# Performance work log

Hardware: AMD Instinct MI355X
Metric: run time of the kernel (lower is better)

## Reference

```python
import jax, jax.numpy as jnp
import numpy as np

N = 16384          # tokens (batch*seq)
D = 2048           # input_dim
H = 2 * D          # router hidden dim
E = 64             # num_experts
NUM_SHARED = 8
TOP_K = 2


def setup_inputs() -> dict:
    key = jax.random.key(0)
    k_x, k_w1, k_b1, k_w2, k_b2 = jax.random.split(key, 5)
    s1 = 1.0 / np.sqrt(D)
    s2 = 1.0 / np.sqrt(H)
    return {
        "x": jax.random.normal(k_x, (N, D), dtype=jnp.float32),
        "W1": jax.random.uniform(k_w1, (D, H), jnp.float32, -s1, s1),
        "b1": jax.random.uniform(k_b1, (H,), jnp.float32, -s1, s1),
        "W2": jax.random.uniform(k_w2, (H, E), jnp.float32, -s2, s2),
        "b2": jax.random.uniform(k_b2, (E,), jnp.float32, -s2, s2),
    }


def reference(x, W1, b1, W2, b2):
    # router MLP: linear -> exact (erf) GELU -> linear -> softmax
    h = jax.nn.gelu(x @ W1 + b1, approximate=False)          # [N, H]
    weights = jax.nn.softmax(h @ W2 + b2, axis=-1)            # [N, E]
    global_weights = weights[:, :NUM_SHARED]                  # [N, num_shared]
    local = weights[:, NUM_SHARED:]                           # [N, E - num_shared]
    local_weights, local_indices = jax.lax.top_k(local, TOP_K)  # [N, top_k] each
    return (global_weights, local_weights, local_indices, weights)
```

## Files before the change

### kernel.cpp

```cpp
#include <hip/hip_runtime.h>
#include <math.h>

namespace {
constexpr int kN = 16384;
constexpr int kD = 2048;
constexpr int kH = 4096;
constexpr int kE = 64;
constexpr int kShared = 8;

constexpr int OFF_GW = 0;
constexpr int OFF_LW = kN * kShared;
constexpr int OFF_LI = OFF_LW + kN * 2;
constexpr int OFF_W  = OFF_LI + kN * 2;

constexpr int GS_STRIDE = 132;
constexpr int HSPLIT = 4;
constexpr int CHUNKS = 8;

constexpr size_t XH_OFF  = 0;
constexpr size_t XL_OFF  = (size_t)kN * kD;
constexpr size_t W1TH_OFF = XL_OFF + (size_t)kN * kD;
constexpr size_t W1TL_OFF = W1TH_OFF + (size_t)kH * kD;
constexpr size_t WS_BASE = (W1TL_OFF + (size_t)kH * kD) * 2;
constexpr size_t PART_FLOAT_OFF = WS_BASE / 4;
constexpr size_t WS_FULL = WS_BASE + (size_t)HSPLIT * kN * kE * 4;

constexpr int BUF_FLOATS = 64 * GS_STRIDE;
constexpr int BUF_F16    = BUF_FLOATS * 2;

constexpr int CXB = 8192;
}

typedef _Float16 half8  __attribute__((ext_vector_type(8)));
typedef _Float16 half4t __attribute__((ext_vector_type(4)));
typedef float    f32x16 __attribute__((ext_vector_type(16)));

__device__ __forceinline__ void async16(const _Float16* g, _Float16* l) {
    __builtin_amdgcn_global_load_lds(
        (const __attribute__((address_space(1))) void*)g,
        (__attribute__((address_space(3))) void*)l, 16, 0, 0);
}

__global__ __launch_bounds__(256)
void convert_xw(const float* __restrict__ x, _Float16* __restrict__ xh,
                _Float16* __restrict__ xl,
                const float* __restrict__ W1, _Float16* __restrict__ th,
                _Float16* __restrict__ tl)
{
    __shared__ float T[64][65];
    const int b = blockIdx.x;
    const int t = threadIdx.x;

    if (b < CXB) {
        #pragma unroll
        for (int it = 0; it < 4; ++it) {
            const size_t i = (((size_t)it * CXB + b) * 256 + t) * 4;
            const float4 v = *reinterpret_cast<const float4*>(x + i);
            half4t h, l;
            const float vs[4] = {v.x, v.y, v.z, v.w};
            #pragma unroll
            for (int j = 0; j < 4; ++j) {
                const _Float16 hj = (_Float16)vs[j];
                h[j] = hj;
                l[j] = (_Float16)((vs[j] - (float)hj) * 2048.0f);
            }
            *reinterpret_cast<half4t*>(xh + i) = h;
            *reinterpret_cast<half4t*>(xl + i) = l;
        }
        return;
    }

    const int bb = b - CXB;
    const int bk = bb & 31;
    const int bn = bb >> 5;
    const int k0 = bk * 64, n0 = bn * 64;
    const int c4 = (t & 15) * 4, r = t >> 4;

    #pragma unroll
    for (int i = 0; i < 4; ++i) {
        const int kk = r + 16 * i;
        const float4 v = *reinterpret_cast<const float4*>(
            W1 + (size_t)(k0 + kk) * kH + n0 + c4);
        T[kk][c4 + 0] = v.x; T[kk][c4 + 1] = v.y;
        T[kk][c4 + 2] = v.z; T[kk][c4 + 3] = v.w;
    }
    __syncthreads();
    #pragma unroll
    for (int i = 0; i < 4; ++i) {
        const int nn = r + 16 * i;
        half4t h, l;
        #pragma unroll
        for (int j = 0; j < 4; ++j) {
            const float vv = T[c4 + j][nn];
            const _Float16 hj = (_Float16)vv;
            h[j] = hj;
            l[j] = (_Float16)((vv - (float)hj) * 2048.0f);
        }
        *reinterpret_cast<half4t*>(th + (size_t)(n0 + nn) * kD + k0 + c4) = h;
        *reinterpret_cast<half4t*>(tl + (size_t)(n0 + nn) * kD + k0 + c4) = l;
    }
}

__global__ __launch_bounds__(256, 2)
void gemm1_mfma(const _Float16* __restrict__ xh, const float* __restrict__ b1,
                const float* __restrict__ W2, float* __restrict__ dst,
                int atomicMode)
{
    __shared__ __align__(16) float smem[2 * BUF_FLOATS];

    const int t = threadIdx.x;
    const int lane = t & 63;
    const int w = t >> 6;
    const int bx = blockIdx.x;
    const int xcd = bx & 7;
    const int j8 = bx >> 3;
    const int hSplit = 2 * (xcd & 1) + (j8 & 1);
    const int rowBlock = (xcd >> 1) * 32 + (j8 >> 1);
    const int rowBase = rowBlock * 128;

    const int mw = (w >> 1) * 64;
    const int nc32 = (w & 1) * 32;

    unsigned int gofsA[4], gofsB[4];
    #pragma unroll
    for (int i = 0; i < 8; ++i) {
        const int c = i * 256 + t;
        const int tile = c >> 9;
        const int s = c & 511;
        const int row = s >> 2;
        const int pq = s & 3;
        const int q = pq ^ (row & 3) ^ ((row >> 2) & 3);
        const unsigned int plane =
            (tile == 0) ? (unsigned int)XH_OFF :
            (tile == 1) ? (unsigned int)XL_OFF :
            (tile == 2) ? (unsigned int)W1TH_OFF : (unsigned int)W1TL_OFF;
        if (tile < 2)
            gofsA[i] = plane + (unsigned int)(rowBase + row) * kD + q * 8;
        else
            gofsB[i - 4] = plane + (unsigned int)row * kD + q * 8;
    }

    int aOff[2][2], bOff[2][2];
    #pragma unroll
    for (int mt = 0; mt < 2; ++mt)
        #pragma unroll
        for (int ks = 0; ks < 2; ++ks) {
            const int row = mw + mt * 32 + (lane & 31);
            const int q = (lane >> 5) + 2 * ks;
            aOff[mt][ks] = row * 32 + ((q ^ (row & 3) ^ ((row >> 2) & 3)) * 8);
        }
    #pragma unroll
    for (int nt = 0; nt < 2; ++nt)
        #pragma unroll
        for (int ks = 0; ks < 2; ++ks) {
            const int row = nt * 64 + nc32 + (lane & 31);
            const int q = (lane >> 5) + 2 * ks;
            bOff[nt][ks] = row * 32 + ((q ^ (row & 3) ^ ((row >> 2) & 3)) * 8);
        }

    const int g_r0 = (t >> 3) * 4;
    const int g_e0 = (t & 7) * 8;
    float lacc[4][8];
    #pragma unroll
    for (int i = 0; i < 4; ++i)
        #pragma unroll
        for (int j = 0; j < 8; ++j) lacc[i][j] = 0.0f;

    auto stageA = [&](int buf, int nk) {
        _Float16* l = (_Float16*)smem + (size_t)buf * BUF_F16;
        #pragma unroll
        for (int i = 0; i < 4; ++i)
            async16(xh + gofsA[i] + nk, l + ((i * 256 + t) * 8));
    };
    auto stageB = [&](int buf, int nc, int nk) {
        _Float16* l = (_Float16*)smem + (size_t)buf * BUF_F16;
        const unsigned int hOff =
            (unsigned int)(hSplit * (CHUNKS * 128) + nc * 128) * kD;
        #pragma unroll
        for (int i = 0; i < 4; ++i)
            async16(xh + gofsB[i] + hOff + nk, l + (((i + 4) * 256 + t) * 8));
    };

    int cur = 0;
    stageA(0, 0);
    stageB(0, 0, 0);

    for (int chunk = 0; chunk < CHUNKS; ++chunk) {
        const int hBase = hSplit * (CHUNKS * 128) + chunk * 128;

        f32x16 accH[2][2], accL[2][2];
        #pragma unroll
        for (int a = 0; a < 2; ++a)
            #pragma unroll
            for (int b = 0; b < 2; ++b)
                #pragma unroll
                for (int r = 0; r < 16; ++r) { accH[a][b][r] = 0.0f; accL[a][b][r] = 0.0f; }

        for (int kt = 0; kt < kD; kt += 32) {
            const bool isLast = (chunk == CHUNKS - 1) && (kt == kD - 32);
            int nc = chunk, nk = kt + 32;
            if (nk == kD) { nc = chunk + 1; nk = 0; }

            const _Float16* lds = (const _Float16*)smem + (size_t)cur * BUF_F16;
            const int nbuf = cur ^ 1;

            if (!isLast) {
                stageA(nbuf, nk);
                asm volatile("s_waitcnt vmcnt(4)" ::: "memory");
            } else {
                asm volatile("s_waitcnt vmcnt(0)" ::: "memory");
            }
            __builtin_amdgcn_s_barrier();
            asm volatile("" ::: "memory");

            {
                half8 aH[2], aL[2], bH[2], bL[2];
                #pragma unroll
                for (int mt = 0; mt < 2; ++mt) {
                    aH[mt] = *reinterpret_cast<const half8*>(lds + aOff[mt][0]);
                    aL[mt] = *reinterpret_cast<const half8*>(lds + 4096 + aOff[mt][0]);
                }
                #pragma unroll
                for (int nt = 0; nt < 2; ++nt) {
                    bH[nt] = *reinterpret_cast<const half8*>(lds + 8192 + bOff[nt][0]);
                    bL[nt] = *reinterpret_cast<const half8*>(lds + 12288 + bOff[nt][0]);
                }
                if (!isLast) stageB(nbuf, nc, nk);
                __builtin_amdgcn_s_setprio(1);
                #pragma unroll
                for (int mt = 0; mt < 2; ++mt)
                    #pragma unroll
                    for (int nt = 0; nt < 2; ++nt) {
                        accH[mt][nt] = __builtin_amdgcn_mfma_f32_32x32x16_f16(
                            aH[mt], bH[nt], accH[mt][nt], 0, 0, 0);
                        accL[mt][nt] = __builtin_amdgcn_mfma_f32_32x32x16_f16(
                            aH[mt], bL[nt], accL[mt][nt], 0, 0, 0);
                        accL[mt][nt] = __builtin_amdgcn_mfma_f32_32x32x16_f16(
                            aL[mt], bH[nt], accL[mt][nt], 0, 0, 0);
                    }
                __builtin_amdgcn_s_setprio(0);
                __builtin_amdgcn_sched_barrier(0);
            }
            asm volatile("" ::: "memory");
            __builtin_amdgcn_s_barrier();
            asm volatile("" ::: "memory");

            {
                half8 aH[2], aL[2], bH[2], bL[2];
                #pragma unroll
                for (int mt = 0; mt < 2; ++mt) {
                    aH[mt] = *reinterpret_cast<const half8*>(lds + aOff[mt][1]);
                    aL[mt] = *reinterpret_cast<const half8*>(lds + 4096 + aOff[mt][1]);
                }
                #pragma unroll
                for (int nt = 0; nt < 2; ++nt) {
                    bH[nt] = *reinterpret_cast<const half8*>(lds + 8192 + bOff[nt][1]);
                    bL[nt] = *reinterpret_cast<const half8*>(lds + 12288 + bOff[nt][1]);
                }
                __builtin_amdgcn_s_setprio(1);
                #pragma unroll
                for (int mt = 0; mt < 2; ++mt)
                    #pragma unroll
                    for (int nt = 0; nt < 2; ++nt) {
                        accH[mt][nt] = __builtin_amdgcn_mfma_f32_32x32x16_f16(
                            aH[mt], bH[nt], accH[mt][nt], 0, 0, 0);
                        accL[mt][nt] = __builtin_amdgcn_mfma_f32_32x32x16_f16(
                            aH[mt], bL[nt], accL[mt][nt], 0, 0, 0);
                        accL[mt][nt] = __builtin_amdgcn_mfma_f32_32x32x16_f16(
                            aL[mt], bH[nt], accL[mt][nt], 0, 0, 0);
                    }
                __builtin_amdgcn_s_setprio(0);
                __builtin_amdgcn_sched_barrier(0);
            }
            asm volatile("s_waitcnt lgkmcnt(0)" ::: "memory");
            __builtin_amdgcn_s_barrier();
            asm volatile("" ::: "memory");
            cur ^= 1;
        }

        float* gS = smem + (size_t)(cur ^ 1) * BUF_FLOATS;
        const float inv2048 = 1.0f / 2048.0f;
        const int hl = nc32 + (lane & 31);
        for (int hf = 0; hf < 2; ++hf) {
            if (hf) {
                asm volatile("s_waitcnt lgkmcnt(0)" ::: "memory");
                __builtin_amdgcn_s_barrier();
                asm volatile("" ::: "memory");
            }
            const float bb = b1[hBase + hf * 64 + hl];
            #pragma unroll
            for (int mt = 0; mt < 2; ++mt) {
                #pragma unroll
                for (int rq = 0; rq < 4; ++rq) {
                    float vr[4];
                    #pragma unroll
                    for (int rr = 0; rr < 4; ++rr) {
                        const int r = rq * 4 + rr;
                        const float hv = accH[mt][hf][r] + accL[mt][hf][r] * inv2048 + bb;
                        vr[rr] = 0.5f * hv * (1.0f + erff(hv * 0.70710678118654752f));
                    }
                    const int mrow = mw + mt * 32 + 8 * rq + 4 * (lane >> 5);
                    *reinterpret_cast<float4*>(gS + hl * GS_STRIDE + mrow) =
                        make_float4(vr[0], vr[1], vr[2], vr[3]);
                }
            }
            asm volatile("s_waitcnt lgkmcnt(0)" ::: "memory");
            __builtin_amdgcn_s_barrier();
            asm volatile("" ::: "memory");
            const float* W2p = W2 + (size_t)(hBase + hf * 64) * kE + g_e0;
            #pragma unroll 4
            for (int h = 0; h < 64; ++h) {
                const float4 gv = *reinterpret_cast<const float4*>(gS + h * GS_STRIDE + g_r0);
                const float4 w0 = *reinterpret_cast<const float4*>(W2p + (size_t)h * kE);
                const float4 w1 = *reinterpret_cast<const float4*>(W2p + (size_t)h * kE + 4);
                const float ga[4] = {gv.x, gv.y, gv.z, gv.w};
                const float wb[8] = {w0.x, w0.y, w0.z, w0.w, w1.x, w1.y, w1.z, w1.w};
                #pragma unroll
                for (int i = 0; i < 4; ++i)
                    #pragma unroll
                    for (int j = 0; j < 8; ++j)
                        lacc[i][j] = fmaf(ga[i], wb[j], lacc[i][j]);
            }
        }
        asm volatile("s_waitcnt lgkmcnt(0)" ::: "memory");
        __builtin_amdgcn_s_barrier();
        asm volatile("" ::: "memory");
    }

    if (atomicMode) {
        #pragma unroll
        for (int i = 0; i < 4; ++i)
            #pragma unroll
            for (int j = 0; j < 8; ++j)
                atomicAdd(dst + (size_t)(rowBase + g_r0 + i) * kE + g_e0 + j, lacc[i][j]);
    } else {
        float* drow = dst + ((size_t)hSplit * kN + rowBase + g_r0) * kE + g_e0;
        #pragma unroll
        for (int i = 0; i < 4; ++i) {
            *reinterpret_cast<float4*>(drow + (size_t)i * kE) =
                make_float4(lacc[i][0], lacc[i][1], lacc[i][2], lacc[i][3]);
            *reinterpret_cast<float4*>(drow + (size_t)i * kE + 4) =
                make_float4(lacc[i][4], lacc[i][5], lacc[i][6], lacc[i][7]);
        }
    }
}

__global__ __launch_bounds__(256, 2)
void gemm1_kernel(const float* __restrict__ x, const float* __restrict__ W1,
                  const float* __restrict__ b1, const float* __restrict__ W2,
                  float* __restrict__ logits)
{
    __shared__ __align__(16) float smem[64 * GS_STRIDE];
    float* As = smem;
    float* Bs = smem + 32 * 128;
    float* gS = smem;

    const int t  = threadIdx.x;
    const int bx = blockIdx.x;
    const int rowBlock = bx >> 2;
    const int hSplit   = bx & 3;
    const int rowBase  = rowBlock * 128;
    const int hBase0   = hSplit * 1024;

    const int ty = t >> 4;
    const int tx = t & 15;
    const int r0 = ty * 8;
    const int c0 = tx * 8;
    const int g_r0 = (t >> 3) * 4;
    const int g_e0 = (t & 7) * 8;

    float lacc[4][8];
    #pragma unroll
    for (int i = 0; i < 4; ++i)
        #pragma unroll
        for (int j = 0; j < 8; ++j) lacc[i][j] = 0.0f;

    for (int chunk = 0; chunk < 8; ++chunk) {
        const int hBase = hBase0 + chunk * 128;
        float C[8][8];
        #pragma unroll
        for (int i = 0; i < 8; ++i)
            #pragma unroll
            for (int j = 0; j < 8; ++j) C[i][j] = 0.0f;

        for (int kt = 0; kt < kD; kt += 32) {
            __syncthreads();
            #pragma unroll
            for (int i = 0; i < 4; ++i) {
                const int f  = t + 256 * i;
                const int m  = f >> 3;
                const int kq = (f & 7) * 4;
                const float4 v = *reinterpret_cast<const float4*>(
                    x + (size_t)(rowBase + m) * kD + kt + kq);
                As[(kq + 0) * 128 + m] = v.x;
                As[(kq + 1) * 128 + m] = v.y;
                As[(kq + 2) * 128 + m] = v.z;
                As[(kq + 3) * 128 + m] = v.w;
            }
            #pragma unroll
            for (int i = 0; i < 4; ++i) {
                const int f  = t + 256 * i;
                const int k  = f >> 5;
                const int n4 = (f & 31) * 4;
                *reinterpret_cast<float4*>(Bs + k * 128 + n4) =
                    *reinterpret_cast<const float4*>(W1 + (size_t)(kt + k) * kH + hBase + n4);
            }
            __syncthreads();
            #pragma unroll 8
            for (int k = 0; k < 32; ++k) {
                const float4 a0 = *reinterpret_cast<const float4*>(As + k * 128 + r0);
                const float4 a1 = *reinterpret_cast<const float4*>(As + k * 128 + r0 + 4);
                const float4 b0 = *reinterpret_cast<const float4*>(Bs + k * 128 + c0);
                const float4 b1v = *reinterpret_cast<const float4*>(Bs + k * 128 + c0 + 4);
                const float a[8] = {a0.x, a0.y, a0.z, a0.w, a1.x, a1.y, a1.z, a1.w};
                const float b[8] = {b0.x, b0.y, b0.z, b0.w, b1v.x, b1v.y, b1v.z, b1v.w};
                #pragma unroll
                for (int i = 0; i < 8; ++i)
                    #pragma unroll
                    for (int j = 0; j < 8; ++j)
                        C[i][j] = fmaf(a[i], b[j], C[i][j]);
            }
        }

        #pragma unroll
        for (int j = 0; j < 8; ++j) {
            const float bb = b1[hBase + c0 + j];
            #pragma unroll
            for (int i = 0; i < 8; ++i) {
                const float hv = C[i][j] + bb;
                C[i][j] = 0.5f * hv * (1.0f + erff(hv * 0.70710678118654752f));
            }
        }

        for (int half = 0; half < 2; ++half) {
            __syncthreads();
            if ((tx >> 3) == half) {
                const int hloc0 = c0 - half * 64;
                #pragma unroll
                for (int j = 0; j < 8; ++j) {
                    const float4 col = make_float4(C[0][j], C[1][j], C[2][j], C[3][j]);
                    const float4 col2 = make_float4(C[4][j], C[5][j], C[6][j], C[7][j]);
                    *reinterpret_cast<float4*>(gS + (hloc0 + j) * GS_STRIDE + r0)     = col;
                    *reinterpret_cast<float4*>(gS + (hloc0 + j) * GS_STRIDE + r0 + 4) = col2;
                }
            }
            __syncthreads();
            const float* W2p = W2 + (size_t)(hBase + half * 64) * kE + g_e0;
            #pragma unroll 4
            for (int h = 0; h < 64; ++h) {
                const float4 gv = *reinterpret_cast<const float4*>(gS + h * GS_STRIDE + g_r0);
                const float4 w0 = *reinterpret_cast<const float4*>(W2p + (size_t)h * kE);
                const float4 w1 = *reinterpret_cast<const float4*>(W2p + (size_t)h * kE + 4);
                const float ga[4] = {gv.x, gv.y, gv.z, gv.w};
                const float wb[8] = {w0.x, w0.y, w0.z, w0.w, w1.x, w1.y, w1.z, w1.w};
                #pragma unroll
                for (int i = 0; i < 4; ++i)
                    #pragma unroll
                    for (int j = 0; j < 8; ++j)
                        lacc[i][j] = fmaf(ga[i], wb[j], lacc[i][j]);
            }
        }
    }

    #pragma unroll
    for (int i = 0; i < 4; ++i)
        #pragma unroll
        for (int j = 0; j < 8; ++j)
            atomicAdd(logits + (size_t)(rowBase + g_r0 + i) * kE + g_e0 + j, lacc[i][j]);
}

__global__ __launch_bounds__(256)
void router_kernel(const float* __restrict__ b2, const float* __restrict__ src,
                   int atomicMode, float* __restrict__ out)
{
    const int lane = threadIdx.x & 63;
    const int row  = blockIdx.x * 4 + (threadIdx.x >> 6);

    float logit;
    if (atomicMode) {
        logit = src[(size_t)row * kE + lane] + b2[lane];
    } else {
        const float* p = src + (size_t)row * kE + lane;
        logit = p[0] + p[(size_t)kN * kE] + p[(size_t)2 * kN * kE] +
                p[(size_t)3 * kN * kE] + b2[lane];
    }

    float m = logit;
    #pragma unroll
    for (int off = 32; off > 0; off >>= 1) m = fmaxf(m, __shfl_xor(m, off));
    const float p = expf(logit - m);
    float s = p;
    #pragma unroll
    for (int off = 32; off > 0; off >>= 1) s += __shfl_xor(s, off);
    const float w = p / s;

    out[OFF_W + (size_t)row * kE + lane] = w;
    if (lane < kShared) out[OFF_GW + (size_t)row * kShared + lane] = w;

    float v1 = (lane >= kShared) ? w : -1.0f;
    int   i1 = lane - kShared;
    #pragma unroll
    for (int off = 32; off > 0; off >>= 1) {
        const float ov = __shfl_xor(v1, off);
        const int   oi = __shfl_xor(i1, off);
        if (ov > v1 || (ov == v1 && oi < i1)) { v1 = ov; i1 = oi; }
    }
    float v2 = (lane >= kShared && (lane - kShared) != i1) ? w : -1.0f;
    int   i2 = lane - kShared;
    #pragma unroll
    for (int off = 32; off > 0; off >>= 1) {
        const float ov = __shfl_xor(v2, off);
        const int   oi = __shfl_xor(i2, off);
        if (ov > v2 || (ov == v2 && oi < i2)) { v2 = ov; i2 = oi; }
    }
    if (lane == 0) {
        out[OFF_LW + (size_t)row * 2 + 0] = v1;
        out[OFF_LW + (size_t)row * 2 + 1] = v2;
        out[OFF_LI + (size_t)row * 2 + 0] = (float)i1;
        out[OFF_LI + (size_t)row * 2 + 1] = (float)i2;
    }
}

extern "C" void kernel_launch(void* const* d_in, const int* in_sizes, int n_in,
                              void* d_out, int out_size, void* d_ws, size_t ws_size,
                              hipStream_t stream)
{
    const float* x  = (const float*)d_in[0];
    const float* W1 = (const float*)d_in[1];
    const float* b1 = (const float*)d_in[2];
    const float* W2 = (const float*)d_in[3];
    const float* b2 = (const float*)d_in[4];
    float* out = (float*)d_out;
    float* logits = out + OFF_W;

    if (ws_size >= WS_BASE) {
        _Float16* base = (_Float16*)d_ws;
        const int atomicMode = (ws_size >= WS_FULL) ? 0 : 1;
        float* dst = atomicMode ? logits : ((float*)d_ws + PART_FLOAT_OFF);
        if (atomicMode)
            hipMemsetAsync(logits, 0, (size_t)kN * kE * sizeof(float), stream);
        hipLaunchKernelGGL(convert_xw, dim3(CXB + (kD / 64) * (kH / 64)), dim3(256), 0, stream,
                           x, base + XH_OFF, base + XL_OFF,
                           W1, base + W1TH_OFF, base + W1TL_OFF);
        hipLaunchKernelGGL(gemm1_mfma, dim3((kN / 128) * HSPLIT), dim3(256), 0, stream,
                           base + XH_OFF, b1, W2, dst, atomicMode);
        hipLaunchKernelGGL(router_kernel, dim3(kN / 4), dim3(256), 0, stream,
                           b2, dst, atomicMode, out);
    } else {
        hipMemsetAsync(logits, 0, (size_t)kN * kE * sizeof(float), stream);
        hipLaunchKernelGGL(gemm1_kernel, dim3((kN / 128) * 4), dim3(256), 0, stream,
                           x, W1, b1, W2, logits);
        hipLaunchKernelGGL(router_kernel, dim3(kN / 4), dim3(256), 0, stream,
                           b2, logits, 1, out);
    }
}
```

Before: 1.225 ms.

## Add dedicated producer wave for async loads and merge split-fp16 accumulators

Adds a fifth wavefront per block that alone issues the async global-to-LDS loads for the double-buffered tiles, so the four compute waves only run MFMAs. The scaling of the split-fp16 operands moves so the hi*hi, hi*lo and lo*hi products all land at one scale, letting a single accumulator replace the separate high and low accumulators. This frees registers, and launch bounds move from 256 threads at 2 blocks to 320 threads at 3 blocks. The risks are that a single producer wave may not keep up with the load rate, and that the extra barrier per k-step and the changed precision scaling (hi scaled by 2048 in fp16, x lo unscaled) could cost throughput or accuracy.

```diff
diff --git a/kernel.cpp b/kernel.cpp
--- a/kernel.cpp
+++ b/kernel.cpp
@@ -62,7 +62,7 @@
             for (int j = 0; j < 4; ++j) {
                 const _Float16 hj = (_Float16)vs[j];
                 h[j] = hj;
-                l[j] = (_Float16)((vs[j] - (float)hj) * 2048.0f);
+                l[j] = (_Float16)(vs[j] - (float)hj);
             }
             *reinterpret_cast<half4t*>(xh + i) = h;
             *reinterpret_cast<half4t*>(xl + i) = l;
@@ -93,7 +93,7 @@
         for (int j = 0; j < 4; ++j) {
             const float vv = T[c4 + j][nn];
             const _Float16 hj = (_Float16)vv;
-            h[j] = hj;
+            h[j] = (_Float16)((float)hj * 2048.0f);
             l[j] = (_Float16)((vv - (float)hj) * 2048.0f);
         }
         *reinterpret_cast<half4t*>(th + (size_t)(n0 + nn) * kD + k0 + c4) = h;
@@ -101,7 +101,7 @@
     }
 }
 
-__global__ __launch_bounds__(256, 2)
+__global__ __launch_bounds__(320, 3)
 void gemm1_mfma(const _Float16* __restrict__ xh, const float* __restrict__ b1,
                 const float* __restrict__ W2, float* __restrict__ dst,
                 int atomicMode)
@@ -111,6 +111,7 @@
     const int t = threadIdx.x;
     const int lane = t & 63;
     const int w = t >> 6;
+    const bool producer = (w == 4);
     const int bx = blockIdx.x;
     const int xcd = bx & 7;
     const int j8 = bx >> 3;
@@ -121,25 +122,6 @@
     const int mw = (w >> 1) * 64;
     const int nc32 = (w & 1) * 32;
 
-    unsigned int gofsA[4], gofsB[4];
-    #pragma unroll
-    for (int i = 0; i < 8; ++i) {
-        const int c = i * 256 + t;
-        const int tile = c >> 9;
-        const int s = c & 511;
-        const int row = s >> 2;
-        const int pq = s & 3;
-        const int q = pq ^ (row & 3) ^ ((row >> 2) & 3);
-        const unsigned int plane =
-            (tile == 0) ? (unsigned int)XH_OFF :
-            (tile == 1) ? (unsigned int)XL_OFF :
-            (tile == 2) ? (unsigned int)W1TH_OFF : (unsigned int)W1TL_OFF;
-        if (tile < 2)
-            gofsA[i] = plane + (unsigned int)(rowBase + row) * kD + q * 8;
-        else
-            gofsB[i - 4] = plane + (unsigned int)row * kD + q * 8;
-    }
-
     int aOff[2][2], bOff[2][2];
     #pragma unroll
     for (int mt = 0; mt < 2; ++mt)
@@ -158,7 +140,7 @@
             bOff[nt][ks] = row * 32 + ((q ^ (row & 3) ^ ((row >> 2) & 3)) * 8);
         }
 
-    const int g_r0 = (t >> 3) * 4;
+    const int g_r0 = ((t & 255) >> 3) * 4;
     const int g_e0 = (t & 7) * 8;
     float lacc[4][8];
     #pragma unroll
@@ -166,160 +148,139 @@
         #pragma unroll
         for (int j = 0; j < 8; ++j) lacc[i][j] = 0.0f;
 
-    auto stageA = [&](int buf, int nk) {
+    const int pr0 = lane >> 2, ppq = lane & 3;
+    auto pstage = [&](int buf, int chunk, int kt) {
         _Float16* l = (_Float16*)smem + (size_t)buf * BUF_F16;
-        #pragma unroll
-        for (int i = 0; i < 4; ++i)
-            async16(xh + gofsA[i] + nk, l + ((i * 256 + t) * 8));
+        const int hBase = hSplit * (CHUNKS * 128) + chunk * 128;
+        #pragma clang loop unroll(disable)
+        for (int i = 0; i < 32; ++i) {
+            const int tile = i >> 3;
+            const int row = (i & 7) * 16 + pr0;
+            const int q = ppq ^ (row & 3) ^ ((row >> 2) & 3);
+            const unsigned int plane =
+                (tile == 0) ? (unsigned int)XH_OFF :
+                (tile == 1) ? (unsigned int)XL_OFF :
+                (tile == 2) ? (unsigned int)W1TH_OFF : (unsigned int)W1TL_OFF;
+            const unsigned int rsel = (tile < 2 ? rowBase : hBase) + row;
+            async16(xh + plane + rsel * (unsigned)kD + q * 8 + kt,
+                    l + ((i * 64 + lane) * 8));
+        }
     };
-    auto stageB = [&](int buf, int nc, int nk) {
-        _Float16* l = (_Float16*)smem + (size_t)buf * BUF_F16;
-        const unsigned int hOff =
-            (unsigned int)(hSplit * (CHUNKS * 128) + nc * 128) * kD;
-        #pragma unroll
-        for (int i = 0; i < 4; ++i)
-            async16(xh + gofsB[i] + hOff + nk, l + (((i + 4) * 256 + t) * 8));
-    };
-
-    int cur = 0;
-    stageA(0, 0);
-    stageB(0, 0, 0);
+
+    const float inv2048 = 1.0f / 2048.0f;
+    const int hl = nc32 + (lane & 31);
 
     for (int chunk = 0; chunk < CHUNKS; ++chunk) {
         const int hBase = hSplit * (CHUNKS * 128) + chunk * 128;
 
-        f32x16 accH[2][2], accL[2][2];
+        f32x16 acc[2][2];
         #pragma unroll
         for (int a = 0; a < 2; ++a)
             #pragma unroll
             for (int b = 0; b < 2; ++b)
                 #pragma unroll
-                for (int r = 0; r < 16; ++r) { accH[a][b][r] = 0.0f; accL[a][b][r] = 0.0f; }
-
-        for (int kt = 0; kt < kD; kt += 32) {
-            const bool isLast = (chunk == CHUNKS - 1) && (kt == kD - 32);
-            int nc = chunk, nk = kt + 32;
-            if (nk == kD) { nc = chunk + 1; nk = 0; }
-
-            const _Float16* lds = (const _Float16*)smem + (size_t)cur * BUF_F16;
-            const int nbuf = cur ^ 1;
-
-            if (!isLast) {
-                stageA(nbuf, nk);
-                asm volatile("s_waitcnt vmcnt(4)" ::: "memory");
-            } else {
-                asm volatile("s_waitcnt vmcnt(0)" ::: "memory");
-            }
-            __builtin_amdgcn_s_barrier();
-            asm volatile("" ::: "memory");
-
-            {
-                half8 aH[2], aL[2], bH[2], bL[2];
-                #pragma unroll
-                for (int mt = 0; mt < 2; ++mt) {
-                    aH[mt] = *reinterpret_cast<const half8*>(lds + aOff[mt][0]);
-                    aL[mt] = *reinterpret_cast<const half8*>(lds + 4096 + aOff[mt][0]);
-                }
-                #pragma unroll
-                for (int nt = 0; nt < 2; ++nt) {
-                    bH[nt] = *reinterpret_cast<const half8*>(lds + 8192 + bOff[nt][0]);
-                    bL[nt] = *reinterpret_cast<const half8*>(lds + 12288 + bOff[nt][0]);
-                }
-                if (!isLast) stageB(nbuf, nc, nk);
-                __builtin_amdgcn_s_setprio(1);
-                #pragma unroll
-                for (int mt = 0; mt < 2; ++mt)
-                    #pragma unroll
-                    for (int nt = 0; nt < 2; ++nt) {
-                        accH[mt][nt] = __builtin_amdgcn_mfma_f32_32x32x16_f16(
-                            aH[mt], bH[nt], accH[mt][nt], 0, 0, 0);
-                        accL[mt][nt] = __builtin_amdgcn_mfma_f32_32x32x16_f16(
-                            aH[mt], bL[nt], accL[mt][nt], 0, 0, 0);
-                        accL[mt][nt] = __builtin_amdgcn_mfma_f32_32x32x16_f16(
-                            aL[mt], bH[nt], accL[mt][nt], 0, 0, 0);
-                    }
-                __builtin_amdgcn_s_setprio(0);
-                __builtin_amdgcn_sched_barrier(0);
-            }
+                for (int r = 0; r < 16; ++r) acc[a][b][r] = 0.0f;
+
+        if (producer) {
+            pstage(0, chunk, 0);
+            pstage(1, chunk, 32);
+            asm volatile("s_waitcnt vmcnt(32)" ::: "memory");
+        }
+
+        for (int s = 0; s < 64; ++s) {
             asm volatile("" ::: "memory");
             __builtin_amdgcn_s_barrier();
             asm volatile("" ::: "memory");
 
-            {
-                half8 aH[2], aL[2], bH[2], bL[2];
-                #pragma unroll
-                for (int mt = 0; mt < 2; ++mt) {
-                    aH[mt] = *reinterpret_cast<const half8*>(lds + aOff[mt][1]);
-                    aL[mt] = *reinterpret_cast<const half8*>(lds + 4096 + aOff[mt][1]);
+            if (!producer) {
+                const _Float16* lds = (const _Float16*)smem + (size_t)(s & 1) * BUF_F16;
+                #pragma unroll
+                for (int ks = 0; ks < 2; ++ks) {
+                    half8 aH[2], aL[2], bH[2], bL[2];
+                    #pragma unroll
+                    for (int mt = 0; mt < 2; ++mt) {
+                        aH[mt] = *reinterpret_cast<const half8*>(lds + aOff[mt][ks]);
+                        aL[mt] = *reinterpret_cast<const half8*>(lds + 4096 + aOff[mt][ks]);
+                    }
+                    #pragma unroll
+                    for (int nt = 0; nt < 2; ++nt) {
+                        bH[nt] = *reinterpret_cast<const half8*>(lds + 8192 + bOff[nt][ks]);
+                        bL[nt] = *reinterpret_cast<const half8*>(lds + 12288 + bOff[nt][ks]);
+                    }
+                    __builtin_amdgcn_s_setprio(1);
+                    #pragma unroll
+                    for (int mt = 0; mt < 2; ++mt)
+                        #pragma unroll
+                        for (int nt = 0; nt < 2; ++nt) {
+                            acc[mt][nt] = __builtin_amdgcn_mfma_f32_32x32x16_f16(
+                                aH[mt], bH[nt], acc[mt][nt], 0, 0, 0);
+                            acc[mt][nt] = __builtin_amdgcn_mfma_f32_32x32x16_f16(
+                                aH[mt], bL[nt], acc[mt][nt], 0, 0, 0);
+                            acc[mt][nt] = __builtin_amdgcn_mfma_f32_32x32x16_f16(
+                                aL[mt], bH[nt], acc[mt][nt], 0, 0, 0);
+                        }
+                    __builtin_amdgcn_s_setprio(0);
                 }
-                #pragma unroll
-                for (int nt = 0; nt < 2; ++nt) {
-                    bH[nt] = *reinterpret_cast<const half8*>(lds + 8192 + bOff[nt][1]);
-                    bL[nt] = *reinterpret_cast<const half8*>(lds + 12288 + bOff[nt][1]);
-                }
-                __builtin_amdgcn_s_setprio(1);
-                #pragma unroll
-                for (int mt = 0; mt < 2; ++mt)
-                    #pragma unroll
-                    for (int nt = 0; nt < 2; ++nt) {
-                        accH[mt][nt] = __builtin_amdgcn_mfma_f32_32x32x16_f16(
-                            aH[mt], bH[nt], accH[mt][nt], 0, 0, 0);
-                        accL[mt][nt] = __builtin_amdgcn_mfma_f32_32x32x16_f16(
-                            aH[mt], bL[nt], accL[mt][nt], 0, 0, 0);
-                        accL[mt][nt] = __builtin_amdgcn_mfma_f32_32x32x16_f16(
-                            aL[mt], bH[nt], accL[mt][nt], 0, 0, 0);
-                    }
-                __builtin_amdgcn_s_setprio(0);
-                __builtin_amdgcn_sched_barrier(0);
-            }
-            asm volatile("s_waitcnt lgkmcnt(0)" ::: "memory");
+            }
+
+            asm volatile("" ::: "memory");
             __builtin_amdgcn_s_barrier();
             asm volatile("" ::: "memory");
-            cur ^= 1;
-        }
-
-        float* gS = smem + (size_t)(cur ^ 1) * BUF_FLOATS;
-        const float inv2048 = 1.0f / 2048.0f;
-        const int hl = nc32 + (lane & 31);
+
+            if (producer) {
+                if (s + 2 < 64) {
+                    pstage(s & 1, chunk, (s + 2) * 32);
+                    asm volatile("s_waitcnt vmcnt(32)" ::: "memory");
+                } else if (s == 62) {
+                    asm volatile("s_waitcnt vmcnt(0)" ::: "memory");
+                }
+            }
+        }
+
+        float* gS = smem;
         for (int hf = 0; hf < 2; ++hf) {
             if (hf) {
                 asm volatile("s_waitcnt lgkmcnt(0)" ::: "memory");
                 __builtin_amdgcn_s_barrier();
                 asm volatile("" ::: "memory");
             }
-            const float bb = b1[hBase + hf * 64 + hl];
-            #pragma unroll
-            for (int mt = 0; mt < 2; ++mt) {
-                #pragma unroll
-                for (int rq = 0; rq < 4; ++rq) {
-                    float vr[4];
-                    #pragma unroll
-                    for (int rr = 0; rr < 4; ++rr) {
-                        const int r = rq * 4 + rr;
-                        const float hv = accH[mt][hf][r] + accL[mt][hf][r] * inv2048 + bb;
-                        vr[rr] = 0.5f * hv * (1.0f + erff(hv * 0.70710678118654752f));
+            if (!producer) {
+                const float bb = b1[hBase + hf * 64 + hl];
+                #pragma unroll
+                for (int mt = 0; mt < 2; ++mt) {
+                    #pragma unroll
+                    for (int rq = 0; rq < 4; ++rq) {
+                        float vr[4];
+                        #pragma unroll
+                        for (int rr = 0; rr < 4; ++rr) {
+                            const int r = rq * 4 + rr;
+                            const float hv = acc[mt][hf][r] * inv2048 + bb;
+                            vr[rr] = 0.5f * hv * (1.0f + erff(hv * 0.70710678118654752f));
+                        }
+                        const int mrow = mw + mt * 32 + 8 * rq + 4 * (lane >> 5);
+                        *reinterpret_cast<float4*>(gS + hl * GS_STRIDE + mrow) =
+                            make_float4(vr[0], vr[1], vr[2], vr[3]);
                     }
-                    const int mrow = mw + mt * 32 + 8 * rq + 4 * (lane >> 5);
-                    *reinterpret_cast<float4*>(gS + hl * GS_STRIDE + mrow) =
-                        make_float4(vr[0], vr[1], vr[2], vr[3]);
                 }
             }
             asm volatile("s_waitcnt lgkmcnt(0)" ::: "memory");
             __builtin_amdgcn_s_barrier();
             asm volatile("" ::: "memory");
-            const float* W2p = W2 + (size_t)(hBase + hf * 64) * kE + g_e0;
-            #pragma unroll 4
-            for (int h = 0; h < 64; ++h) {
-                const float4 gv = *reinterpret_cast<const float4*>(gS + h * GS_STRIDE + g_r0);
-                const float4 w0 = *reinterpret_cast<const float4*>(W2p + (size_t)h * kE);
-                const float4 w1 = *reinterpret_cast<const float4*>(W2p + (size_t)h * kE + 4);
-                const float ga[4] = {gv.x, gv.y, gv.z, gv.w};
-                const float wb[8] = {w0.x, w0.y, w0.z, w0.w, w1.x, w1.y, w1.z, w1.w};
-                #pragma unroll
-                for (int i = 0; i < 4; ++i)
-                    #pragma unroll
-                    for (int j = 0; j < 8; ++j)
-                        lacc[i][j] = fmaf(ga[i], wb[j], lacc[i][j]);
+            if (t < 256) {
+                const float* W2p = W2 + (size_t)(hBase + hf * 64) * kE + g_e0;
+                #pragma unroll 4
+                for (int h = 0; h < 64; ++h) {
+                    const float4 gv = *reinterpret_cast<const float4*>(gS + h * GS_STRIDE + g_r0);
+                    const float4 w0 = *reinterpret_cast<const float4*>(W2p + (size_t)h * kE);
+                    const float4 w1 = *reinterpret_cast<const float4*>(W2p + (size_t)h * kE + 4);
+                    const float ga[4] = {gv.x, gv.y, gv.z, gv.w};
+                    const float wb[8] = {w0.x, w0.y, w0.z, w0.w, w1.x, w1.y, w1.z, w1.w};
+                    #pragma unroll
+                    for (int i = 0; i < 4; ++i)
+                        #pragma unroll
+                        for (int j = 0; j < 8; ++j)
+                            lacc[i][j] = fmaf(ga[i], wb[j], lacc[i][j]);
+                }
             }
         }
         asm volatile("s_waitcnt lgkmcnt(0)" ::: "memory");
@@ -327,20 +288,22 @@
         asm volatile("" ::: "memory");
     }
 
-    if (atomicMode) {
-        #pragma unroll
-        for (int i = 0; i < 4; ++i)
-            #pragma unroll
-            for (int j = 0; j < 8; ++j)
-                atomicAdd(dst + (size_t)(rowBase + g_r0 + i) * kE + g_e0 + j, lacc[i][j]);
-    } else {
-        float* drow = dst + ((size_t)hSplit * kN + rowBase + g_r0) * kE + g_e0;
-        #pragma unroll
-        for (int i = 0; i < 4; ++i) {
-            *reinterpret_cast<float4*>(drow + (size_t)i * kE) =
-                make_float4(lacc[i][0], lacc[i][1], lacc[i][2], lacc[i][3]);
-            *reinterpret_cast<float4*>(drow + (size_t)i * kE + 4) =
-                make_float4(lacc[i][4], lacc[i][5], lacc[i][6], lacc[i][7]);
+    if (t < 256) {
+        if (atomicMode) {
+            #pragma unroll
+            for (int i = 0; i < 4; ++i)
+                #pragma unroll
+                for (int j = 0; j < 8; ++j)
+                    atomicAdd(dst + (size_t)(rowBase + g_r0 + i) * kE + g_e0 + j, lacc[i][j]);
+        } else {
+            float* drow = dst + ((size_t)hSplit * kN + rowBase + g_r0) * kE + g_e0;
+            #pragma unroll
+            for (int i = 0; i < 4; ++i) {
+                *reinterpret_cast<float4*>(drow + (size_t)i * kE) =
+                    make_float4(lacc[i][0], lacc[i][1], lacc[i][2], lacc[i][3]);
+                *reinterpret_cast<float4*>(drow + (size_t)i * kE + 4) =
+                    make_float4(lacc[i][4], lacc[i][5], lacc[i][6], lacc[i][7]);
+            }
         }
     }
 }
@@ -542,7 +505,7 @@
         hipLaunchKernelGGL(convert_xw, dim3(CXB + (kD / 64) * (kH / 64)), dim3(256), 0, stream,
                            x, base + XH_OFF, base + XL_OFF,
                            W1, base + W1TH_OFF, base + W1TL_OFF);
-        hipLaunchKernelGGL(gemm1_mfma, dim3((kN / 128) * HSPLIT), dim3(256), 0, stream,
+        hipLaunchKernelGGL(gemm1_mfma, dim3((kN / 128) * HSPLIT), dim3(320), 0, stream,
                            base + XH_OFF, b1, W2, dst, atomicMode);
         hipLaunchKernelGGL(router_kernel, dim3(kN / 4), dim3(256), 0, stream,
                            b2, dst, atomicMode, out);
```

After: 3.133 ms. 2.56x slower.
